# Performance work log

Measured on AMD Instinct MI355X. Metric: run time of the kernel, lower is better.

Reference implementation:

```python
import jax, jax.numpy as jnp
import numpy as np

V = 32000   # vocab_size
S = 4096    # seq_len
D = 1024    # dim
H = 4096    # hidden_dim
L = 2       # num_layers
CS = 64     # chunk_size
R = 256     # low_rank_dim = max(8, D//4)
WIN = 8     # window_size (OptitationLayer default)
NEG = -1e30


def setup_inputs() -> dict:
    key = jax.random.key(0)
    ks = jax.random.split(key, 20)
    f32 = jnp.float32
    inp = {}
    inp['idx_seq'] = jax.random.randint(ks[0], (S,), 0, V)
    inp['embeddings'] = jax.random.normal(ks[1], (V, D), f32) * 0.01
    inp['positional'] = jax.random.normal(ks[2], (S, D), f32) * 0.01
    # per-layer MLP params, stacked over layer axis
    inp['Wg'] = jax.random.normal(ks[3], (L, D, D), f32) / D ** 0.5
    inp['bg'] = jnp.zeros((L, D), f32)
    inp['Ws'] = jax.random.normal(ks[4], (L, D, H), f32) / D ** 0.5
    inp['bs'] = jnp.zeros((L, H), f32)
    inp['Wo'] = jax.random.normal(ks[5], (L, H, D), f32) / H ** 0.5
    inp['bo'] = jnp.zeros((L, D), f32)
    # per-layer optitation (windowed attention) params
    inp['Wq'] = jax.random.normal(ks[6], (L, D, R), f32) / D ** 0.5
    inp['Wk'] = jax.random.normal(ks[7], (L, D, R), f32) / D ** 0.5
    inp['Wv'] = jax.random.normal(ks[8], (L, D, R), f32) / D ** 0.5
    inp['Wao'] = jax.random.normal(ks[9], (L, R, D), f32) / R ** 0.5
    inp['bq'] = jnp.zeros((L, R), f32)
    inp['bk'] = jnp.zeros((L, R), f32)
    inp['bv'] = jnp.zeros((L, R), f32)
    inp['bao'] = jnp.zeros((L, D), f32)
    inp['outW'] = jax.random.normal(ks[10], (D, V), f32) / D ** 0.5
    inp['outb'] = jnp.zeros((V,), f32)
    return inp


def _optitation(x, Wq, bq, Wk, bk, Wv, bv, Wao, bao):
    Q = x @ Wq + bq
    K = x @ Wk + bk
    Vv = x @ Wv + bv
    s = x.shape[0]
    off = jnp.arange(WIN + 1)
    j = jnp.arange(s)[:, None] - off[None, :]  # [s, w+1] key indices
    valid = j >= 0
    jc = jnp.maximum(j, 0)
    Kw = K[jc]   # [s, w+1, R]
    Vw = Vv[jc]  # [s, w+1, R]
    scores = jnp.einsum('sr,swr->sw', Q, Kw) / jnp.sqrt(jnp.float32(R))
    scores = jnp.where(valid, scores, NEG)
    attn = jax.nn.softmax(scores, axis=-1)
    ao = jnp.einsum('sw,swr->sr', attn, Vw)   # [s, R]
    return ao @ Wao + bao


def _chunk_link(x):
    # chunk-averaging with half-weighted neighbor chunks
    s, d = x.shape
    pad = (-s) % CS
    xp = jnp.pad(x, ((0, pad), (0, 0)))
    n = xp.shape[0] // CS
    c = xp.reshape(n, CS, d)
    prev = jnp.concatenate([jnp.zeros_like(c[:1]), c[:-1]], axis=0)
    nxt = jnp.concatenate([c[1:], jnp.zeros_like(c[:1])], axis=0)
    i = jnp.arange(n)
    w = 1.0 + 0.5 * (i > 0).astype(x.dtype) + 0.5 * (i < n - 1).astype(x.dtype)
    upd = (c + 0.5 * prev + 0.5 * nxt) / w[:, None, None]
    return upd.reshape(-1, d)[:s]


def reference(idx_seq, embeddings, positional, Wg, bg, Ws, bs, Wo, bo,
              Wq, bq, Wk, bk, Wv, bv, Wao, bao, outW, outb):
    s = idx_seq.shape[0]
    x = embeddings[idx_seq] + positional[:s]
    # decay accumulation: x[pos] += 0.8**pos * x[0] for pos >= 1 (x[0] untouched)
    decay = jnp.power(jnp.float32(0.8), jnp.arange(s, dtype=jnp.float32))
    decay = decay.at[0].set(0.0)
    x = x + decay[:, None] * x[0]
    for l in range(L):
        residual = x
        x = x * jax.nn.sigmoid(x @ Wg[l] + bg[l])            # lensed gate
        x = jnp.tanh(x @ Ws[l] + bs[l]) @ Wo[l] + bo[l]       # context sculpt
        x = x + residual
        x = x + _optitation(x, Wq[l], bq[l], Wk[l], bk[l],
                            Wv[l], bv[l], Wao[l], bao[l])
        x = _chunk_link(x)
    return x @ outW + outb
```

## Files before the change

### kernel.cpp

```cpp
#include <hip/hip_runtime.h>
#include <hip/hip_bf16.h>
#include <math.h>

#define S_LEN 4096
#define DIM   1024
#define HID   4096
#define NLAYER 2
#define RDIM  256
#define VOCAB 32000
#define QKVN  768

typedef unsigned short u16;
typedef __attribute__((ext_vector_type(8))) short s16x8;
typedef __attribute__((ext_vector_type(4))) float f32x4;
typedef __attribute__((ext_vector_type(4))) unsigned short u16x4;

__device__ inline u16 f2b(float f){
  unsigned u = __float_as_uint(f);
  u += 0x7fff + ((u >> 16) & 1);
  return (u16)(u >> 16);
}

__device__ inline void gload_lds16(const void* g, void* l){
  __builtin_amdgcn_global_load_lds((__attribute__((address_space(1))) void*)(g),
                                   (__attribute__((address_space(3))) void*)(l), 16, 0, 0);
}

__global__ void k_prep(const float* __restrict__ Wg,  const float* __restrict__ Ws,
                       const float* __restrict__ Wo,  const float* __restrict__ Wq,
                       const float* __restrict__ Wk,  const float* __restrict__ Wv,
                       const float* __restrict__ Wao, const float* __restrict__ outW,
                       u16* __restrict__ WgT, u16* __restrict__ WsT, u16* __restrict__ WoT,
                       u16* __restrict__ WqkvT, u16* __restrict__ WaoT, u16* __restrict__ outWT,
                       const float* __restrict__ bq, const float* __restrict__ bk,
                       const float* __restrict__ bv, float* __restrict__ bqkv2){
  __shared__ float tile[64][65];
  int tx = threadIdx.x, ty = threadIdx.y;
  int id = blockIdx.x;
  if (id < 6){
    int t = ty * 16 + tx;
    int l = id / 3, sel = id % 3;
    const float* s = sel == 0 ? bq : (sel == 1 ? bk : bv);
    bqkv2[l * 768 + sel * 256 + t] = s[(size_t)l * 256 + t];
    return;
  }
  id -= 6;
  const float* src; u16* dst; int K, N, bx, by;
  if (id < 512){
    int z = id >> 8, lo = id & 255;
    src = Wg + (size_t)z * DIM * DIM; dst = WgT + (size_t)z * DIM * DIM;
    K = DIM; N = DIM; bx = lo & 15; by = lo >> 4;
  } else if (id < 2560){
    int local = id - 512; int z = local >> 10, lo = local & 1023;
    src = Ws + (size_t)z * DIM * HID; dst = WsT + (size_t)z * DIM * HID;
    K = DIM; N = HID; bx = lo & 63; by = lo >> 6;
  } else if (id < 4608){
    int local = id - 2560; int z = local >> 10, lo = local & 1023;
    src = Wo + (size_t)z * HID * DIM; dst = WoT + (size_t)z * HID * DIM;
    K = HID; N = DIM; bx = lo & 15; by = lo >> 4;
  } else if (id < 4736){
    int local = id - 4608; int z = local >> 6, lo = local & 63;
    src = Wq + (size_t)z * DIM * RDIM; dst = WqkvT + (size_t)z * QKVN * DIM;
    K = DIM; N = RDIM; bx = lo & 3; by = lo >> 2;
  } else if (id < 4864){
    int local = id - 4736; int z = local >> 6, lo = local & 63;
    src = Wk + (size_t)z * DIM * RDIM; dst = WqkvT + (size_t)z * QKVN * DIM + (size_t)256 * DIM;
    K = DIM; N = RDIM; bx = lo & 3; by = lo >> 2;
  } else if (id < 4992){
    int local = id - 4864; int z = local >> 6, lo = local & 63;
    src = Wv + (size_t)z * DIM * RDIM; dst = WqkvT + (size_t)z * QKVN * DIM + (size_t)512 * DIM;
    K = DIM; N = RDIM; bx = lo & 3; by = lo >> 2;
  } else if (id < 5120){
    int local = id - 4992; int z = local >> 6, lo = local & 63;
    src = Wao + (size_t)z * RDIM * DIM; dst = WaoT + (size_t)z * RDIM * DIM;
    K = RDIM; N = DIM; bx = lo & 15; by = lo >> 4;
  } else {
    int local = id - 5120;
    src = outW; dst = outWT;
    K = DIM; N = VOCAB; bx = local % 500; by = local / 500;
  }
  int n0 = bx * 64, k0 = by * 64;
  #pragma unroll
  for (int i = 0; i < 4; i++){
    float4 v = *(const float4*)&src[(size_t)(k0 + ty + 16 * i) * N + n0 + tx * 4];
    tile[ty + 16 * i][tx * 4 + 0] = v.x;
    tile[ty + 16 * i][tx * 4 + 1] = v.y;
    tile[ty + 16 * i][tx * 4 + 2] = v.z;
    tile[ty + 16 * i][tx * 4 + 3] = v.w;
  }
  __syncthreads();
  #pragma unroll
  for (int i = 0; i < 4; i++){
    u16x4 o;
    #pragma unroll
    for (int j = 0; j < 4; j++) o[j] = f2b(tile[tx * 4 + j][ty + 16 * i]);
    *(u16x4*)&dst[(size_t)(n0 + ty + 16 * i) * K + k0 + tx * 4] = o;
  }
}

__global__ void k_embed(const int* __restrict__ idx, const float* __restrict__ emb,
                        const float* __restrict__ pos, float* __restrict__ xf,
                        u16* __restrict__ xb){
  int s = blockIdx.x;
  int d = blockIdx.y * 256 + threadIdx.x;
  float v = emb[(size_t)idx[s] * DIM + d] + pos[(size_t)s * DIM + d];
  if (s > 0){
    float x0 = emb[(size_t)idx[0] * DIM + d] + pos[d];
    v += exp2f((float)s * -0.3219280948873623f) * x0;
  }
  size_t o = (size_t)s * DIM + d;
  xf[o] = v; xb[o] = f2b(v);
}

#define EP_GATE  0
#define EP_TANH  1
#define EP_RESID 2
#define EP_BIASF 3
#define EP_AO    4
#define EP_OUT   5

#define PH_SYNC() do{ asm volatile("" ::: "memory"); __builtin_amdgcn_s_barrier(); asm volatile("" ::: "memory"); }while(0)


#define MMA_QUAD(MH, NLO, BF) \
  { _Pragma("unroll") for (int mi = 0; mi < 4; mi++){ \
    _Pragma("unroll") for (int ni = 0; ni < 2; ni++){ \
      _Pragma("unroll") for (int ks = 0; ks < 2; ks++){ \
        acc[(MH)*4+mi][(NLO)+ni] = __builtin_amdgcn_mfma_f32_16x16x32_bf16((BF)[ni*2+ks], af[mi*2+ks], acc[(MH)*4+mi][(NLO)+ni], 0, 0, 0); } } } }

#define LDA(MH, BO) \
  { _Pragma("unroll") for (int mi = 0; mi < 4; mi++){ \
    _Pragma("unroll") for (int ks = 0; ks < 2; ks++){ \
      af[mi*2+ks] = *(const s16x8*)(pa0 + (BO) + ((MH)*4+mi)*1024 + ((ks ^ kb) * 32)); } } }

#define LDB(NH, BO) \
  { _Pragma("unroll") for (int ni = 0; ni < 2; ni++){ \
    _Pragma("unroll") for (int ks = 0; ks < 2; ks++){ \
      bf_[(NH)*4+ni*2+ks] = *(const s16x8*)(pb0 + (BO) + ((NH)*2+ni)*1024 + ((ks ^ kb) * 32)); } } }

__global__ __launch_bounds__(512, 2) void k_gemmL(
    const u16* __restrict__ A, const u16* __restrict__ Bt,
    const float* __restrict__ bias, float* __restrict__ outf,
    int N, int K, int tilesM, int tilesN){
  extern __shared__ u16 lds[];
  const int t = threadIdx.x;
  const int w = t >> 6, l = t & 63;
  const int wr = w >> 2, wc = w & 3;
  const int NT = K >> 6;
  const int NI = NT >> 1;
  const int nTiles = tilesM * tilesN;

  const int r0 = t >> 3;
  const int scol = (((t & 7) ^ ((t >> 3) & 7)) * 8);
  const int cb = (((l >> 4) ^ (l & 3)) * 8);
  const int kb = (l >> 2) & 1;
  const u16* pa0 = lds + (wr * 128 + (l & 15)) * 64 + cb;
  const u16* pb0 = lds + 32768 + (wc * 64 + (l & 15)) * 64 + cb;

  auto decode = [&](int idx, int& bR, int& bC){
    int pr = tilesN * 2;
    int stripe = idx / pr, r2 = idx % pr;
    bR = (stripe * 2 + (r2 & 1)) * 256;
    bC = (r2 >> 1) * 256;
  };

  int startT = (int)(((long long)blockIdx.x * nTiles) / gridDim.x);
  int endT   = (int)(((long long)(blockIdx.x + 1) * nTiles) / gridDim.x);
  if (startT >= endT) return;
  int tileIdx = startT;
  int bRow, bCol, nRow = 0, nCol = 0;
  bool hasNext = false;
  decode(tileIdx, bRow, bCol);

  auto stage_half = [&](int tau, int q){
    const u16* base;
    if (tau >= NT){
      if (!hasNext) return;
      tau -= NT;
      base = (q < 2) ? A + (size_t)nRow * K : Bt + (size_t)nCol * K;
    } else {
      base = (q < 2) ? A + (size_t)bRow * K : Bt + (size_t)bCol * K;
    }
    int h = q & 1;
    const u16* gp = base + (size_t)(h * 128 + r0) * K + (size_t)tau * 64 + scol;
    u16* d = lds + ((q < 2) ? 0 : 32768) + ((tau & 1) * 16384) + h * 8192 + t * 8;
    gload_lds16(gp, d);
    gload_lds16(gp + (size_t)64 * K, d + 4096);
  };

  f32x4 acc[8][4] = {};
  s16x8 af[8], bf_[8];

  stage_half(0, 0); stage_half(0, 1); stage_half(0, 2); stage_half(0, 3);
  stage_half(1, 0);
  asm volatile("s_waitcnt vmcnt(2)" ::: "memory");
  PH_SYNC();

  for (; tileIdx < endT; ++tileIdx){
    hasNext = (tileIdx + 1) < endT;
    if (hasNext) decode(tileIdx + 1, nRow, nCol);

    for (int i = 0; i < NI; i++){
      const int t1 = 2 * i + 1, t2 = 2 * i + 2, t3 = 2 * i + 3;
      const bool lastGate = (!hasNext) && (i + 1 == NI);
      LDA(0, 0); LDB(0, 0);
      stage_half(t1, 1);
      PH_SYNC();
      __builtin_amdgcn_s_setprio(1); MMA_QUAD(0, 0, bf_); __builtin_amdgcn_s_setprio(0);
      PH_SYNC();
      LDB(1, 0);
      stage_half(t1, 2);
      PH_SYNC();
      __builtin_amdgcn_s_setprio(1); MMA_QUAD(0, 2, bf_ + 4); __builtin_amdgcn_s_setprio(0);
      PH_SYNC();
      LDA(1, 0);
      stage_half(t1, 3);
      PH_SYNC();
      __builtin_amdgcn_s_setprio(1); MMA_QUAD(1, 2, bf_ + 4); __builtin_amdgcn_s_setprio(0);
      PH_SYNC();
      stage_half(t2, 0);
      if (!lastGate) asm volatile("s_waitcnt vmcnt(2)" ::: "memory");
      else           asm volatile("s_waitcnt vmcnt(0)" ::: "memory");
      PH_SYNC();
      __builtin_amdgcn_s_setprio(1); MMA_QUAD(1, 0, bf_); __builtin_amdgcn_s_setprio(0);
      PH_SYNC();
      LDA(0, 16384); LDB(0, 16384);
      stage_half(t2, 1);
      PH_SYNC();
      __builtin_amdgcn_s_setprio(1); MMA_QUAD(0, 0, bf_); __builtin_amdgcn_s_setprio(0);
      PH_SYNC();
      LDB(1, 16384);
      stage_half(t2, 2);
      PH_SYNC();
      __builtin_amdgcn_s_setprio(1); MMA_QUAD(0, 2, bf_ + 4); __builtin_amdgcn_s_setprio(0);
      PH_SYNC();
      LDA(1, 16384);
      stage_half(t2, 3);
      PH_SYNC();
      __builtin_amdgcn_s_setprio(1); MMA_QUAD(1, 2, bf_ + 4); __builtin_amdgcn_s_setprio(0);
      PH_SYNC();
      stage_half(t3, 0);
      if (!lastGate) asm volatile("s_waitcnt vmcnt(2)" ::: "memory");
      PH_SYNC();
      __builtin_amdgcn_s_setprio(1); MMA_QUAD(1, 0, bf_); __builtin_amdgcn_s_setprio(0);
      PH_SYNC();
    }

    #pragma unroll
    for (int m = 0; m < 8; m++){
      int gr = bRow + wr * 128 + m * 16 + (l & 15);
      #pragma unroll
      for (int n = 0; n < 4; n++){
        int gc = bCol + wc * 64 + n * 16 + ((l >> 4) * 4);
        f32x4 v = acc[m][n] + *(const f32x4*)(bias + gc);
        *(f32x4*)(outf + (size_t)gr * N + gc) = v;
        acc[m][n] = (f32x4){0.f, 0.f, 0.f, 0.f};
      }
    }
    bRow = nRow; bCol = nCol;
  }
}


#define MMA2(MH, NL) \
  { _Pragma("unroll") for (int mi = 0; mi < 2; mi++){ \
    _Pragma("unroll") for (int ks = 0; ks < 2; ks++){ \
      acc[(MH)*2+mi][(NL)] = __builtin_amdgcn_mfma_f32_16x16x32_bf16(bf_[(NL)*2+ks], af[mi*2+ks], acc[(MH)*2+mi][(NL)], 0, 0, 0); } } }

#define LDA2(MH, BO) \
  { _Pragma("unroll") for (int mi = 0; mi < 2; mi++){ \
    _Pragma("unroll") for (int ks = 0; ks < 2; ks++){ \
      af[mi*2+ks] = *(const s16x8*)(pa0 + (BO) + ((MH)*2+mi)*1024 + ((ks ^ kb) * 32)); } } }

#define LDB2(NL, BO) \
  { _Pragma("unroll") for (int ks = 0; ks < 2; ks++){ \
    bf_[(NL)*2+ks] = *(const s16x8*)(pb0 + (BO) + (NL)*1024 + ((ks ^ kb) * 32)); } }

template<int EPI>
__global__ __launch_bounds__(512, 4) void k_gemm8b(
    const u16* __restrict__ A, const u16* __restrict__ Bt,
    const float* __restrict__ bias, const float* __restrict__ aux,
    float* __restrict__ outf, u16* __restrict__ outbf,
    int N, int K, int tilesM, int tilesN){
  extern __shared__ u16 lds[];
  const int t = threadIdx.x;
  const int w = t >> 6, l = t & 63;
  const int wr = w >> 2, wc = w & 3;
  const int NT = K >> 6;
  const int NI = NT >> 1;

  int nwg = tilesM * tilesN;
  int id = blockIdx.x, id2;
  if ((nwg & 7) == 0){ int c = nwg >> 3; id2 = (id & 7) * c + (id >> 3); }
  else id2 = id;
  int per = tilesM << 3;
  int g = id2 / per, r = id2 % per;
  int bm = r % tilesM;
  int bn = (g << 3) + r / tilesM;
  const int bRow = bm * 128, bCol = bn * 128;

  const int r0 = t >> 3;
  const int scol = (((t & 7) ^ ((t >> 3) & 7)) * 8);

  auto stage_half = [&](int tau, int q){
    if (tau >= NT) return;
    int h = q & 1;
    bool isA = q < 2;
    const u16* gp = (isA ? A + (size_t)bRow * K : Bt + (size_t)bCol * K)
                 + (size_t)(h * 64 + r0) * K + (size_t)tau * 64 + scol;
    u16* d = lds + (isA ? 0 : 16384) + ((tau & 1) * 8192) + h * 4096 + t * 8;
    gload_lds16(gp, d);
  };

  const int cb = (((l >> 4) ^ (l & 3)) * 8);
  const int kb = (l >> 2) & 1;
  const u16* pa0 = lds + wr * 4096 + (l & 15) * 64 + cb;
  const u16* pb0 = lds + 16384 + (wc >> 1) * 4096 + ((wc & 1) * 32 + (l & 15)) * 64 + cb;

  f32x4 acc[4][2] = {};
  s16x8 af[4], bf_[4];

  stage_half(0, 0); stage_half(0, 1); stage_half(0, 2); stage_half(0, 3);
  stage_half(1, 0);
  asm volatile("s_waitcnt vmcnt(1)" ::: "memory");
  PH_SYNC();

  for (int i = 0; i < NI; i++){
    const int t1 = 2 * i + 1, t2 = 2 * i + 2, t3 = 2 * i + 3;
    const bool last = (i + 1 == NI);
    LDA2(0, 0); LDB2(0, 0);
    stage_half(t1, 1);
    PH_SYNC();
    __builtin_amdgcn_s_setprio(1); MMA2(0, 0); __builtin_amdgcn_s_setprio(0);
    PH_SYNC();
    LDB2(1, 0);
    stage_half(t1, 2);
    PH_SYNC();
    __builtin_amdgcn_s_setprio(1); MMA2(0, 1); __builtin_amdgcn_s_setprio(0);
    PH_SYNC();
    LDA2(1, 0);
    stage_half(t1, 3);
    PH_SYNC();
    __builtin_amdgcn_s_setprio(1); MMA2(1, 1); __builtin_amdgcn_s_setprio(0);
    PH_SYNC();
    stage_half(t2, 0);
    if (!last) asm volatile("s_waitcnt vmcnt(1)" ::: "memory");
    else       asm volatile("s_waitcnt vmcnt(0)" ::: "memory");
    PH_SYNC();
    __builtin_amdgcn_s_setprio(1); MMA2(1, 0); __builtin_amdgcn_s_setprio(0);
    PH_SYNC();
    LDA2(0, 8192); LDB2(0, 8192);
    stage_half(t2, 1);
    PH_SYNC();
    __builtin_amdgcn_s_setprio(1); MMA2(0, 0); __builtin_amdgcn_s_setprio(0);
    PH_SYNC();
    LDB2(1, 8192);
    stage_half(t2, 2);
    PH_SYNC();
    __builtin_amdgcn_s_setprio(1); MMA2(0, 1); __builtin_amdgcn_s_setprio(0);
    PH_SYNC();
    LDA2(1, 8192);
    stage_half(t2, 3);
    PH_SYNC();
    __builtin_amdgcn_s_setprio(1); MMA2(1, 1); __builtin_amdgcn_s_setprio(0);
    PH_SYNC();
    stage_half(t3, 0);
    if (!last) asm volatile("s_waitcnt vmcnt(1)" ::: "memory");
    PH_SYNC();
    __builtin_amdgcn_s_setprio(1); MMA2(1, 0); __builtin_amdgcn_s_setprio(0);
    PH_SYNC();
  }

  #pragma unroll
  for (int m = 0; m < 4; m++){
    int gr = bRow + wr * 64 + m * 16 + (l & 15);
    #pragma unroll
    for (int n = 0; n < 2; n++){
      int gc = bCol + wc * 32 + n * 16 + ((l >> 4) * 4);
      size_t o = (size_t)gr * N + gc;
      f32x4 v = acc[m][n] + *(const f32x4*)(bias + gc);
      if constexpr (EPI == EP_GATE){
        f32x4 a = *(const f32x4*)(aux + o);
        u16x4 rr;
        #pragma unroll
        for (int q = 0; q < 4; q++) rr[q] = f2b(a[q] / (1.f + expf(-v[q])));
        *(u16x4*)(outbf + o) = rr;
      } else if constexpr (EPI == EP_TANH){
        u16x4 rr;
        #pragma unroll
        for (int q = 0; q < 4; q++) rr[q] = f2b(tanhf(v[q]));
        *(u16x4*)(outbf + o) = rr;
      } else if constexpr (EPI == EP_RESID){
        v += *(const f32x4*)(aux + o);
        *(f32x4*)(outf + o) = v;
        u16x4 rr;
        #pragma unroll
        for (int q = 0; q < 4; q++) rr[q] = f2b(v[q]);
        *(u16x4*)(outbf + o) = rr;
      } else if constexpr (EPI == EP_BIASF){
        *(f32x4*)(outf + o) = v;
      } else if constexpr (EPI == EP_AO){
        v += *(const f32x4*)(aux + o);
        *(f32x4*)(outf + o) = v;
      } else {
        *(f32x4*)(outf + o) = v;
      }
    }
  }
}

__global__ void k_attn(const float* __restrict__ qkv, u16* __restrict__ aob){
  int s = blockIdx.x * 4 + (threadIdx.x >> 6);
  int l = threadIdx.x & 63;
  const float* qp = qkv + (size_t)s * QKVN;
  float qr[4];
  #pragma unroll
  for (int r = 0; r < 4; r++) qr[r] = qp[l + 64 * r];
  float sc[9];
  float mx = -1e30f;
  #pragma unroll
  for (int j = 0; j <= 8; j++){
    int sj = s - j;
    bool ok = sj >= 0;
    int row = ok ? sj : 0;
    const float* kp = qkv + (size_t)row * QKVN + RDIM;
    float p = 0.f;
    #pragma unroll
    for (int r = 0; r < 4; r++) p += qr[r] * kp[l + 64 * r];
    #pragma unroll
    for (int off = 32; off; off >>= 1) p += __shfl_xor(p, off);
    p = ok ? p * 0.0625f : -1e30f;
    sc[j] = p;
    mx = fmaxf(mx, p);
  }
  float den = 0.f;
  #pragma unroll
  for (int j = 0; j <= 8; j++){ sc[j] = expf(sc[j] - mx); den += sc[j]; }
  float inv = 1.f / den;
  #pragma unroll
  for (int r = 0; r < 4; r++){
    float a = 0.f;
    #pragma unroll
    for (int j = 0; j <= 8; j++){
      int sj = s - j;
      int row = sj >= 0 ? sj : 0;
      a += sc[j] * qkv[(size_t)row * QKVN + 512 + l + 64 * r];
    }
    aob[(size_t)s * RDIM + l + 64 * r] = f2b(a * inv);
  }
}

__global__ void k_chunk(const float* __restrict__ xin, float* __restrict__ xout,
                        u16* __restrict__ xb){
  int s = blockIdx.x;
  int d = blockIdx.y * 256 + threadIdx.x;
  int ci = s >> 6;
  float v = xin[(size_t)s * DIM + d];
  float wsum = 1.f;
  if (ci > 0){ v += 0.5f * xin[(size_t)(s - 64) * DIM + d]; wsum += 0.5f; }
  if (ci < 63){ v += 0.5f * xin[(size_t)(s + 64) * DIM + d]; wsum += 0.5f; }
  v /= wsum;
  size_t o = (size_t)s * DIM + d;
  xout[o] = v; xb[o] = f2b(v);
}

extern "C" void kernel_launch(void* const* d_in, const int* in_sizes, int n_in,
                              void* d_out, int out_size, void* d_ws, size_t ws_size,
                              hipStream_t stream){
  const int*   idx  = (const int*)d_in[0];
  const float* emb  = (const float*)d_in[1];
  const float* pos  = (const float*)d_in[2];
  const float* Wg   = (const float*)d_in[3];
  const float* bg   = (const float*)d_in[4];
  const float* Ws_  = (const float*)d_in[5];
  const float* bs   = (const float*)d_in[6];
  const float* Wo   = (const float*)d_in[7];
  const float* bo   = (const float*)d_in[8];
  const float* Wq   = (const float*)d_in[9];
  const float* Wk   = (const float*)d_in[10];
  const float* Wv   = (const float*)d_in[11];
  const float* Wao  = (const float*)d_in[12];
  const float* bq   = (const float*)d_in[13];
  const float* bk   = (const float*)d_in[14];
  const float* bv   = (const float*)d_in[15];
  const float* bao  = (const float*)d_in[16];
  const float* outW = (const float*)d_in[17];
  const float* outb = (const float*)d_in[18];
  float* out = (float*)d_out;

  char* p = (char*)d_ws;
  auto alloc = [&](size_t n)->char*{ char* r = p; p += (n + 255) & ~(size_t)255; return r; };
  float* xfA  = (float*)alloc((size_t)S_LEN * DIM * 4);
  float* xfB  = (float*)alloc((size_t)S_LEN * DIM * 4);
  u16*   xb   = (u16*)  alloc((size_t)S_LEN * DIM * 2);
  u16*   xgb  = (u16*)  alloc((size_t)S_LEN * DIM * 2);
  u16*   tbuf = (u16*)  alloc((size_t)S_LEN * HID * 2);
  float* qkvf = (float*)alloc((size_t)S_LEN * QKVN * 4);
  u16*   aob  = (u16*)  alloc((size_t)S_LEN * RDIM * 2);
  float* bqkv2= (float*)alloc(2 * QKVN * 4);
  u16*   WgT  = (u16*)  alloc((size_t)NLAYER * DIM * DIM * 2);
  u16*   WsT  = (u16*)  alloc((size_t)NLAYER * DIM * HID * 2);
  u16*   WoT  = (u16*)  alloc((size_t)NLAYER * HID * DIM * 2);
  u16*   WqkvT= (u16*)  alloc((size_t)NLAYER * QKVN * DIM * 2);
  u16*   WaoT = (u16*)  alloc((size_t)NLAYER * RDIM * DIM * 2);
  u16*   outWT= (u16*)  alloc((size_t)VOCAB * DIM * 2);

  (void)hipFuncSetAttribute((const void*)&k_gemmL,
                      hipFuncAttributeMaxDynamicSharedMemorySize, 131072);
  (void)hipFuncSetAttribute((const void*)&k_gemm8b<EP_GATE>,
                      hipFuncAttributeMaxDynamicSharedMemorySize, 65536);
  (void)hipFuncSetAttribute((const void*)&k_gemm8b<EP_TANH>,
                      hipFuncAttributeMaxDynamicSharedMemorySize, 65536);
  (void)hipFuncSetAttribute((const void*)&k_gemm8b<EP_RESID>,
                      hipFuncAttributeMaxDynamicSharedMemorySize, 65536);
  (void)hipFuncSetAttribute((const void*)&k_gemm8b<EP_BIASF>,
                      hipFuncAttributeMaxDynamicSharedMemorySize, 65536);
  (void)hipFuncSetAttribute((const void*)&k_gemm8b<EP_AO>,
                      hipFuncAttributeMaxDynamicSharedMemorySize, 65536);

  k_prep<<<13126, dim3(16, 16), 0, stream>>>(Wg, Ws_, Wo, Wq, Wk, Wv, Wao, outW,
                                             WgT, WsT, WoT, WqkvT, WaoT, outWT,
                                             bq, bk, bv, bqkv2);

  k_embed<<<dim3(S_LEN, DIM/256), 256, 0, stream>>>(idx, emb, pos, xfA, xb);

  float* curF = xfA; float* altF = xfB;
  for (int l = 0; l < NLAYER; l++){
    k_gemm8b<EP_GATE ><<<(S_LEN/128)*(DIM/128),  512, 65536, stream>>>(xb,  WgT  + (size_t)l*DIM*DIM,  bg + (size_t)l*DIM, curF, nullptr, xgb, DIM, DIM, S_LEN/128, DIM/128);
    k_gemm8b<EP_TANH ><<<(S_LEN/128)*(HID/128),  512, 65536, stream>>>(xgb, WsT  + (size_t)l*DIM*HID,  bs + (size_t)l*HID, nullptr, nullptr, tbuf, HID, DIM, S_LEN/128, HID/128);
    k_gemm8b<EP_RESID><<<(S_LEN/128)*(DIM/128),  512, 65536, stream>>>(tbuf,WoT  + (size_t)l*HID*DIM,  bo + (size_t)l*DIM, curF, curF, xb, DIM, HID, S_LEN/128, DIM/128);
    k_gemm8b<EP_BIASF><<<(S_LEN/128)*(QKVN/128), 512, 65536, stream>>>(xb,  WqkvT + (size_t)l*QKVN*DIM, bqkv2 + (size_t)l*QKVN, nullptr, qkvf, nullptr, QKVN, DIM, S_LEN/128, QKVN/128);
    k_attn<<<S_LEN/4, 256, 0, stream>>>(qkvf, aob);
    k_gemm8b<EP_AO   ><<<(S_LEN/128)*(DIM/128),  512, 65536, stream>>>(aob, WaoT + (size_t)l*RDIM*DIM, bao + (size_t)l*DIM, curF, curF, nullptr, DIM, RDIM, S_LEN/128, DIM/128);
    k_chunk<<<dim3(S_LEN, DIM/256), 256, 0, stream>>>(curF, altF, xb);
    float* tmp = curF; curF = altF; altF = tmp;
  }
  k_gemmL<<<256, 512, 131072, stream>>>(xb, outWT, outb, out, VOCAB, DIM, S_LEN/256, VOCAB/256);
}
```

Baseline: 861.5 us.

## Stride persistent GEMM tiles and prefetch next tile's operands during epilogue

The persistent 256x256 bf16 GEMM now hands out tiles round-robin (tile += gridDim) instead of as contiguous ranges per block. The second k-stage of the next tile is issued before the output-store epilogue, so those loads overlap the stores; the matching loads in the first iteration of the next tile are then skipped, with a looser vmcnt wait. Bias values are loaded once per tile into registers before the k-loop. The hand-tuned vmcnt(34) count is fragile, and the round-robin order changes L2 locality of the tile sequence.

```diff
diff --git a/kernel.cpp b/kernel.cpp
--- a/kernel.cpp
+++ b/kernel.cpp
@@ -164,12 +164,11 @@
     bC = (r2 >> 1) * 256;
   };
 
-  int startT = (int)(((long long)blockIdx.x * nTiles) / gridDim.x);
-  int endT   = (int)(((long long)(blockIdx.x + 1) * nTiles) / gridDim.x);
-  if (startT >= endT) return;
-  int tileIdx = startT;
+  int tileIdx = blockIdx.x;
+  if (tileIdx >= nTiles) return;
   int bRow, bCol, nRow = 0, nCol = 0;
   bool hasNext = false;
+  bool pre = false;
   decode(tileIdx, bRow, bCol);
 
   auto stage_half = [&](int tau, int q){
@@ -196,31 +195,39 @@
   asm volatile("s_waitcnt vmcnt(2)" ::: "memory");
   PH_SYNC();
 
-  for (; tileIdx < endT; ++tileIdx){
-    hasNext = (tileIdx + 1) < endT;
-    if (hasNext) decode(tileIdx + 1, nRow, nCol);
+  for (; tileIdx < nTiles; tileIdx += gridDim.x){
+    int nIdx = tileIdx + gridDim.x;
+    hasNext = nIdx < nTiles;
+    if (hasNext) decode(nIdx, nRow, nCol);
+
+    f32x4 bv4[4];
+    #pragma unroll
+    for (int n = 0; n < 4; n++)
+      bv4[n] = *(const f32x4*)(bias + bCol + wc * 64 + n * 16 + ((l >> 4) * 4));
 
     for (int i = 0; i < NI; i++){
       const int t1 = 2 * i + 1, t2 = 2 * i + 2, t3 = 2 * i + 3;
       const bool lastGate = (!hasNext) && (i + 1 == NI);
+      const bool skipE = pre && (i == 0);
       LDA(0, 0); LDB(0, 0);
-      stage_half(t1, 1);
+      if (!skipE) stage_half(t1, 1);
       PH_SYNC();
       __builtin_amdgcn_s_setprio(1); MMA_QUAD(0, 0, bf_); __builtin_amdgcn_s_setprio(0);
       PH_SYNC();
       LDB(1, 0);
-      stage_half(t1, 2);
+      if (!skipE) stage_half(t1, 2);
       PH_SYNC();
       __builtin_amdgcn_s_setprio(1); MMA_QUAD(0, 2, bf_ + 4); __builtin_amdgcn_s_setprio(0);
       PH_SYNC();
       LDA(1, 0);
-      stage_half(t1, 3);
+      if (!skipE) stage_half(t1, 3);
       PH_SYNC();
       __builtin_amdgcn_s_setprio(1); MMA_QUAD(1, 2, bf_ + 4); __builtin_amdgcn_s_setprio(0);
       PH_SYNC();
       stage_half(t2, 0);
-      if (!lastGate) asm volatile("s_waitcnt vmcnt(2)" ::: "memory");
-      else           asm volatile("s_waitcnt vmcnt(0)" ::: "memory");
+      if (lastGate)      asm volatile("s_waitcnt vmcnt(0)" ::: "memory");
+      else if (skipE)    asm volatile("s_waitcnt vmcnt(34)" ::: "memory");
+      else               asm volatile("s_waitcnt vmcnt(2)" ::: "memory");
       PH_SYNC();
       __builtin_amdgcn_s_setprio(1); MMA_QUAD(1, 0, bf_); __builtin_amdgcn_s_setprio(0);
       PH_SYNC();
@@ -245,6 +252,11 @@
       __builtin_amdgcn_s_setprio(1); MMA_QUAD(1, 0, bf_); __builtin_amdgcn_s_setprio(0);
       PH_SYNC();
     }
+
+    stage_half(NT + 1, 1);
+    stage_half(NT + 1, 2);
+    stage_half(NT + 1, 3);
+    asm volatile("" ::: "memory");
 
     #pragma unroll
     for (int m = 0; m < 8; m++){
@@ -252,15 +264,15 @@
       #pragma unroll
       for (int n = 0; n < 4; n++){
         int gc = bCol + wc * 64 + n * 16 + ((l >> 4) * 4);
-        f32x4 v = acc[m][n] + *(const f32x4*)(bias + gc);
+        f32x4 v = acc[m][n] + bv4[n];
         *(f32x4*)(outf + (size_t)gr * N + gc) = v;
         acc[m][n] = (f32x4){0.f, 0.f, 0.f, 0.f};
       }
     }
+    pre = true;
     bRow = nRow; bCol = nCol;
   }
 }
-
 
 #define MMA2(MH, NL) \
   { _Pragma("unroll") for (int mi = 0; mi < 2; mi++){ \
```

Result: faster. 839.9 us (-2.5%).
